# Optimization experiments

Measured on AMD Instinct MI355X. Metric: run time of the kernel, lower is better.

Reference implementation:

```python
import jax, jax.numpy as jnp
import numpy as np

D_MODEL = 2048
NUM_HEADS = 16
D_K = D_MODEL // NUM_HEADS


def setup_inputs() -> dict:
    key = jax.random.key(0)
    ks = jax.random.split(key, 9)
    s = 1.0 / np.sqrt(D_MODEL)
    return {
        "x": jax.random.normal(ks[0], (2, 2048, D_MODEL), dtype=jnp.float32),
        "Wq": jax.random.normal(ks[1], (D_MODEL, D_MODEL), dtype=jnp.float32) * s,
        "bq": jax.random.normal(ks[2], (D_MODEL,), dtype=jnp.float32) * 0.01,
        "Wk": jax.random.normal(ks[3], (D_MODEL, D_MODEL), dtype=jnp.float32) * s,
        "bk": jax.random.normal(ks[4], (D_MODEL,), dtype=jnp.float32) * 0.01,
        "Wv": jax.random.normal(ks[5], (D_MODEL, D_MODEL), dtype=jnp.float32) * s,
        "bv": jax.random.normal(ks[6], (D_MODEL,), dtype=jnp.float32) * 0.01,
        "Wo": jax.random.normal(ks[7], (D_MODEL, D_MODEL), dtype=jnp.float32) * s,
        "bo": jax.random.normal(ks[8], (D_MODEL,), dtype=jnp.float32) * 0.01,
    }


def reference(x, Wq, bq, Wk, bk, Wv, bv, Wo, bo):
    B, T, C = x.shape
    H, Dk = NUM_HEADS, D_K
    # projections (torch Linear: y = x @ W^T + b; here weights stored as [in,out])
    q = (x @ Wq + bq).reshape(B, T, H, Dk).transpose(0, 2, 1, 3)  # [B,H,T,Dk]
    k = (x @ Wk + bk).reshape(B, T, H, Dk).transpose(0, 2, 1, 3)
    v = (x @ Wv + bv).reshape(B, T, H, Dk).transpose(0, 2, 1, 3)
    score = jnp.einsum("bhqd,bhkd->bhqk", q, k) / jnp.sqrt(jnp.float32(Dk))
    attn = jax.nn.softmax(score, axis=-1)
    out = jnp.einsum("bhqk,bhkd->bhqd", attn, v)  # [B,H,T,Dk]
    out = out.transpose(0, 2, 1, 3).reshape(B, T, C)
    return out @ Wo + bo
```

## Files before the change

kernel.cpp:

```cpp
#include <hip/hip_runtime.h>
#include <cstdint>

typedef _Float16 f16;
typedef __attribute__((ext_vector_type(4))) _Float16 f16x4;
typedef __attribute__((ext_vector_type(8))) _Float16 f16x8;
typedef __attribute__((ext_vector_type(4))) float f32x4;

#define DM   2048
#define TSEQ 2048
#define NB   2
#define NH   16
#define DKH  128
#define LOG2E 1.44269504088896f

__device__ __forceinline__ void gload_lds16(const void* g, void* l) {
  __builtin_amdgcn_global_load_lds((const __attribute__((address_space(1))) void*)g,
                                   (__attribute__((address_space(3))) void*)l, 16, 0, 0);
}

#define SBAR()   asm volatile("s_barrier" ::: "memory")
#define LGKM0()  { asm volatile("s_waitcnt lgkmcnt(0)" ::: "memory"); __builtin_amdgcn_sched_barrier(0); }
#define LGKM8()  asm volatile("s_waitcnt lgkmcnt(8)" ::: "memory")
#define VMCNT4() asm volatile("s_waitcnt vmcnt(4)" ::: "memory")

__global__ __launch_bounds__(256) void cvt_kernel(const float* __restrict__ src,
                                                  f16* __restrict__ dst, int n8) {
  int i = blockIdx.x * 256 + threadIdx.x;
  if (i >= n8) return;
  const float4* s = (const float4*)src + 2 * (size_t)i;
  float4 a = s[0], b = s[1];
  f16x8 o;
  o[0]=(f16)a.x; o[1]=(f16)a.y; o[2]=(f16)a.z; o[3]=(f16)a.w;
  o[4]=(f16)b.x; o[5]=(f16)b.y; o[6]=(f16)b.z; o[7]=(f16)b.w;
  ((f16x8*)dst)[i] = o;
}

__global__ __launch_bounds__(256) void wt_kernel(const float* __restrict__ W0, const float* __restrict__ W1,
                                                 const float* __restrict__ W2, const float* __restrict__ W3,
                                                 f16* __restrict__ Dqkv, f16* __restrict__ Dout) {
  __shared__ f16 S[64 * 80];
  int z = blockIdx.z;
  const float* W = (z == 0) ? W0 : (z == 1) ? W1 : (z == 2) ? W2 : W3;
  f16* D = (z < 3) ? (Dqkv + (size_t)z * DM * DM) : Dout;
  int n0 = blockIdx.x * 64, k0 = blockIdx.y * 64;
  int tid = threadIdx.x;
#pragma unroll
  for (int i = 0; i < 4; i++) {
    int flat = i * 256 + tid;
    int r = flat >> 4, c4 = flat & 15;
    float4 v = *(const float4*)(W + (size_t)(k0 + r) * DM + n0 + c4 * 4);
    S[(c4 * 4 + 0) * 80 + r] = (f16)v.x;
    S[(c4 * 4 + 1) * 80 + r] = (f16)v.y;
    S[(c4 * 4 + 2) * 80 + r] = (f16)v.z;
    S[(c4 * 4 + 3) * 80 + r] = (f16)v.w;
  }
  __syncthreads();
#pragma unroll
  for (int i = 0; i < 2; i++) {
    int flat = i * 256 + tid;
    int nl = flat >> 3, kc = flat & 7;
    f16x8 v = *(const f16x8*)&S[nl * 80 + kc * 8];
    *(f16x8*)(D + (size_t)(n0 + nl) * DM + k0 + kc * 8) = v;
  }
}

template <int MODE>
__global__ __launch_bounds__(512, 2) void gemm_kernel(const f16* __restrict__ A, const f16* __restrict__ Bt,
                                                      const float* __restrict__ b0, const float* __restrict__ b1,
                                                      const float* __restrict__ b2,
                                                      f16* __restrict__ Oh, float* __restrict__ Of) {
  __shared__ __align__(16) f16 As[2][256 * 64];
  __shared__ __align__(16) f16 Bs[2][256 * 64];
  const int K = DM;
  const int NT = K / 64;
  const int NITER = NT / 2;
  constexpr int CPX = (MODE == 0) ? 48 : 16;
  int tid = threadIdx.x, l = tid & 63, w = tid >> 6;
  int lo = l & 15, hi = l >> 4;
  int wm = w >> 2, wn = w & 3;
  int lin = blockIdx.x;
  int swz = (lin & 7) * CPX + (lin >> 3);
  int by = swz & 15, bx = swz >> 4;
  int m0 = by * 256, n0 = bx * 256;

  const f16* Ag = A + (size_t)m0 * K;
  const f16* Bg = Bt + (size_t)n0 * K;

  auto stageA = [&](int b, int h, int t) {
#pragma unroll
    for (int i = 0; i < 2; i++) {
      int flat = i * 512 + tid;
      int row = flat >> 3, c = flat & 7;
      int csw = c ^ (row & 7);
      gload_lds16(Ag + (size_t)(h * 128 + row) * K + t * 64 + csw * 8,
                  &As[b][h * 8192 + i * 4096 + w * 512]);
    }
  };
  auto stageB = [&](int b, int h, int t) {
#pragma unroll
    for (int i = 0; i < 2; i++) {
      int flat = i * 512 + tid;
      int row = flat >> 3, c = flat & 7;
      int csw = c ^ (row & 7);
      gload_lds16(Bg + (size_t)(h * 128 + row) * K + t * 64 + csw * 8,
                  &Bs[b][h * 8192 + i * 4096 + w * 512]);
    }
  };

  f32x4 acc[8][4] = {};
  f16x8 bfr[4][2];
  f16x8 af[2][2];

#define READ_BFRAGS(b)                                                              \
  {                                                                                 \
    _Pragma("unroll")                                                               \
    for (int ni = 0; ni < 4; ni++) {                                                \
      int row = wn * 64 + ni * 16 + lo;                                             \
      bfr[ni][0] = *(const f16x8*)&Bs[b][row * 64 + (((0 + hi) ^ (row & 7)) << 3)]; \
      bfr[ni][1] = *(const f16x8*)&Bs[b][row * 64 + (((4 + hi) ^ (row & 7)) << 3)]; \
    }                                                                               \
  }

#define READ_AFRAGS(b, q)                                                           \
  {                                                                                 \
    _Pragma("unroll")                                                               \
    for (int e = 0; e < 2; e++) {                                                   \
      int row = wm * 128 + ((q) * 2 + e) * 16 + lo;                                 \
      af[e][0] = *(const f16x8*)&As[b][row * 64 + (((0 + hi) ^ (row & 7)) << 3)];   \
      af[e][1] = *(const f16x8*)&As[b][row * 64 + (((4 + hi) ^ (row & 7)) << 3)];   \
    }                                                                               \
  }

#define MFMA_Q(q)                                                                   \
    __builtin_amdgcn_s_setprio(1);                                                  \
    _Pragma("unroll")                                                               \
    for (int e = 0; e < 2; e++)                                                     \
      _Pragma("unroll")                                                             \
      for (int ni = 0; ni < 4; ni++) {                                              \
        acc[(q)*2+e][ni] = __builtin_amdgcn_mfma_f32_16x16x32_f16(af[e][0], bfr[ni][0], acc[(q)*2+e][ni], 0, 0, 0); \
        acc[(q)*2+e][ni] = __builtin_amdgcn_mfma_f32_16x16x32_f16(af[e][1], bfr[ni][1], acc[(q)*2+e][ni], 0, 0, 0); \
      }                                                                             \
    __builtin_amdgcn_s_setprio(0);

  stageB(0, 0, 0); stageB(0, 1, 0);
  stageA(0, 0, 0); stageA(0, 1, 0);
  stageB(1, 0, 1); stageB(1, 1, 1);
  VMCNT4();
  SBAR();

#pragma unroll 1
  for (int it = 0; it < NITER; ++it) {
    int T1 = 2 * it + 1;
    int t2 = (2 * it + 2 < NT) ? 2 * it + 2 : NT - 1;
    int t3 = (2 * it + 3 < NT) ? 2 * it + 3 : NT - 1;

    {
      READ_BFRAGS(0); READ_AFRAGS(0, 0);
      stageA(1, 0, T1);
      LGKM8();
      SBAR(); LGKM0(); MFMA_Q(0); SBAR();
    }
    {
      READ_AFRAGS(0, 1);
      stageA(1, 1, T1); stageB(0, 0, t2);
      SBAR(); LGKM0(); MFMA_Q(1); SBAR();
    }
    {
      READ_AFRAGS(0, 2);
      stageB(0, 1, t2);
      SBAR(); LGKM0(); MFMA_Q(2); SBAR();
    }
    {
      READ_AFRAGS(0, 3);
      SBAR(); LGKM0(); MFMA_Q(3);
      VMCNT4();
      SBAR();
    }
    {
      READ_BFRAGS(1); READ_AFRAGS(1, 0);
      stageA(0, 0, t2);
      LGKM8();
      SBAR(); LGKM0(); MFMA_Q(0); SBAR();
    }
    {
      READ_AFRAGS(1, 1);
      stageA(0, 1, t2);
      SBAR(); LGKM0(); MFMA_Q(1); SBAR();
    }
    {
      READ_AFRAGS(1, 2);
      stageB(1, 0, t3);
      SBAR(); LGKM0(); MFMA_Q(2); SBAR();
    }
    {
      READ_AFRAGS(1, 3);
      stageB(1, 1, t3);
      SBAR(); LGKM0(); MFMA_Q(3);
      VMCNT4();
      SBAR();
    }
  }
  asm volatile("s_waitcnt vmcnt(0)" ::: "memory");

#pragma unroll
  for (int mi = 0; mi < 8; mi++) {
    int gm = m0 + wm * 128 + mi * 16 + (hi << 2);
#pragma unroll
    for (int ni = 0; ni < 4; ni++) {
      int gn = n0 + wn * 64 + ni * 16 + lo;
      if (MODE == 0) {
        int proj = gn >> 11, nn = gn & 2047;
        const float* bp = (proj == 0) ? b0 : (proj == 1) ? b1 : b2;
        float bias = bp[nn];
        int h = nn >> 7, d = nn & 127;
        int b = gm >> 11;
        int t0 = gm & 2047;
        if (proj < 2) {
#pragma unroll
          for (int r = 0; r < 4; r++) {
            Oh[(size_t)proj * ((size_t)NB * NH * TSEQ * DKH) +
               (((size_t)(b * NH + h) * TSEQ + t0 + r) * DKH) + d] = (f16)(acc[mi][ni][r] + bias);
          }
        } else {
          f16x4 pk;
#pragma unroll
          for (int r = 0; r < 4; r++) pk[r] = (f16)(acc[mi][ni][r] + bias);
          *(f16x4*)(Oh + 2ull * ((size_t)NB * NH * TSEQ * DKH) +
                    ((size_t)(b * NH + h) * DKH + d) * TSEQ + t0) = pk;
        }
      } else {
        float bias = b0[gn];
#pragma unroll
        for (int r = 0; r < 4; r++)
          Of[(size_t)(gm + r) * DM + gn] = acc[mi][ni][r] + bias;
      }
    }
  }
#undef READ_BFRAGS
#undef READ_AFRAGS
#undef MFMA_Q
}

__global__ __launch_bounds__(256, 2) void attn_kernel(const f16* __restrict__ Qb, const f16* __restrict__ Kb,
                                                      const f16* __restrict__ Vtb, f16* __restrict__ AO) {
  __shared__ f16 Ks[64 * 128];
  __shared__ f16 Vt[128 * 64];
  __shared__ f16 Ps[4][32 * 72];
  int tid = threadIdx.x, l = tid & 63, w = tid >> 6;
  int lo = l & 15, hi = l >> 4;
  int lin = blockIdx.x;
  int xcd = lin & 7, slot = lin >> 3;
  int bh = xcd * 4 + (slot & 3), qt = slot >> 2;
  const float CSC = 0.12753257f;
  const float THR = 62.0f;
  const f16* Qg = Qb + (size_t)bh * TSEQ * DKH;
  const f16* Kg = Kb + (size_t)bh * TSEQ * DKH;
  const f16* Vg = Vtb + (size_t)bh * DKH * TSEQ;

  f16x8 aq[2][4];
#pragma unroll
  for (int hf = 0; hf < 2; hf++) {
    int qrow = qt * 128 + w * 32 + hf * 16 + lo;
#pragma unroll
    for (int c = 0; c < 4; c++)
      aq[hf][c] = *(const f16x8*)(Qg + (size_t)qrow * DKH + c * 32 + (hi << 3));
  }

  f32x4 o[2][8] = {};
  float mrow[2] = {-INFINITY, -INFINITY};
  float lrow[2] = {0.f, 0.f};

  for (int ktile = 0; ktile < TSEQ / 64; ++ktile) {
    __syncthreads();
#pragma unroll
    for (int i = 0; i < 4; i++) {
      int chunk = (w * 4 + i) * 64 + l;
      int rowk = chunk >> 4, c = chunk & 15;
      int csw = c ^ (rowk & 15);
      gload_lds16(Kg + (size_t)(ktile * 64 + rowk) * DKH + csw * 8, &Ks[(w * 4 + i) * 512]);
    }
#pragma unroll
    for (int i = 0; i < 4; i++) {
      int chunk = (w * 4 + i) * 64 + l;
      int d = chunk >> 3, c = chunk & 7;
      int csw = c ^ (d & 7);
      gload_lds16(Vg + (size_t)d * TSEQ + ktile * 64 + csw * 8, &Vt[(w * 4 + i) * 512]);
    }
    __syncthreads();

    f32x4 s[2][4] = {};
    __builtin_amdgcn_s_setprio(1);
#pragma unroll
    for (int ks = 0; ks < 4; ++ks) {
      int ktl = ks * 16 + lo;
#pragma unroll
      for (int c = 0; c < 4; c++) {
        int cc = (c * 4 + hi) ^ lo;
        f16x8 bk = *(const f16x8*)&Ks[ktl * 128 + cc * 8];
        s[0][ks] = __builtin_amdgcn_mfma_f32_16x16x32_f16(bk, aq[0][c], s[0][ks], 0, 0, 0);
        s[1][ks] = __builtin_amdgcn_mfma_f32_16x16x32_f16(bk, aq[1][c], s[1][ks], 0, 0, 0);
      }
    }
    __builtin_amdgcn_s_setprio(0);

#pragma unroll
    for (int hf = 0; hf < 2; hf++) {
      float mk[4];
#pragma unroll
      for (int ks = 0; ks < 4; ks++)
        mk[ks] = fmaxf(fmaxf(s[hf][ks][0], s[hf][ks][1]), fmaxf(s[hf][ks][2], s[hf][ks][3]));
      float mt = fmaxf(fmaxf(mk[0], mk[1]), fmaxf(mk[2], mk[3]));
      mt = fmaxf(mt, __shfl_xor(mt, 16));
      mt = fmaxf(mt, __shfl_xor(mt, 32));

      if (__any(mt > mrow[hf] + THR)) {
        float mn = fmaxf(mrow[hf], mt);
        float al = exp2f((mrow[hf] - mn) * CSC);
        mrow[hf] = mn;
        lrow[hf] *= al;
        float alr[4];
#pragma unroll
        for (int r = 0; r < 4; r++) alr[r] = __shfl(al, (hi << 2) + r);
#pragma unroll
        for (int dsub = 0; dsub < 8; dsub++)
#pragma unroll
          for (int r = 0; r < 4; r++) o[hf][dsub][r] *= alr[r];
      }

      float mCn = -mrow[hf] * CSC;
      float sum = 0.f;
#pragma unroll
      for (int ks = 0; ks < 4; ks++) {
        f16x4 pk;
        float part = 0.f;
#pragma unroll
        for (int r = 0; r < 4; r++) {
          float p = exp2f(__builtin_fmaf(s[hf][ks][r], CSC, mCn));
          pk[r] = (f16)p;
          part += p;
        }
        sum += part;
        *(f16x4*)&Ps[w][(hf * 16 + lo) * 72 + ks * 16 + (hi << 2)] = pk;
      }
      sum += __shfl_xor(sum, 16);
      sum += __shfl_xor(sum, 32);
      lrow[hf] += sum;
    }

    f16x8 pa[2][2];
#pragma unroll
    for (int hf = 0; hf < 2; hf++)
#pragma unroll
      for (int kk = 0; kk < 2; kk++)
        pa[hf][kk] = *(const f16x8*)&Ps[w][(hf * 16 + lo) * 72 + kk * 32 + (hi << 3)];
    __builtin_amdgcn_s_setprio(1);
#pragma unroll
    for (int kk = 0; kk < 2; kk++) {
#pragma unroll
      for (int dsub = 0; dsub < 8; dsub++) {
        int d = dsub * 16 + lo;
        f16x8 vf = *(const f16x8*)&Vt[d * 64 + (((kk * 4 + hi) ^ (d & 7)) << 3)];
        o[0][dsub] = __builtin_amdgcn_mfma_f32_16x16x32_f16(pa[0][kk], vf, o[0][dsub], 0, 0, 0);
        o[1][dsub] = __builtin_amdgcn_mfma_f32_16x16x32_f16(pa[1][kk], vf, o[1][dsub], 0, 0, 0);
      }
    }
    __builtin_amdgcn_s_setprio(0);
  }

  int b = bh >> 4, h = bh & 15;
#pragma unroll
  for (int hf = 0; hf < 2; hf++) {
    float inv = 1.0f / lrow[hf];
    float invr[4];
#pragma unroll
    for (int r = 0; r < 4; r++) invr[r] = __shfl(inv, (hi << 2) + r);
#pragma unroll
    for (int r = 0; r < 4; r++) {
      int t = qt * 128 + w * 32 + hf * 16 + (hi << 2) + r;
      f16* dst = AO + ((size_t)b * TSEQ + t) * DM + h * DKH;
#pragma unroll
      for (int dsub = 0; dsub < 8; dsub++)
        dst[dsub * 16 + lo] = (f16)(o[hf][dsub][r] * invr[r]);
    }
  }
}

extern "C" void kernel_launch(void* const* d_in, const int* in_sizes, int n_in,
                              void* d_out, int out_size, void* d_ws, size_t ws_size,
                              hipStream_t stream) {
  const float* x  = (const float*)d_in[0];
  const float* Wq = (const float*)d_in[1];
  const float* bq = (const float*)d_in[2];
  const float* Wk = (const float*)d_in[3];
  const float* bk = (const float*)d_in[4];
  const float* Wv = (const float*)d_in[5];
  const float* bv = (const float*)d_in[6];
  const float* Wo = (const float*)d_in[7];
  const float* bo = (const float*)d_in[8];

  f16* ws    = (f16*)d_ws;
  f16* xb    = ws;
  f16* WtQKV = ws + 8388608ull;
  f16* WtO   = ws + 20971520ull;
  f16* Q     = ws + 25165824ull;
  f16* Kp    = ws + 33554432ull;
  f16* Vp    = ws + 41943040ull;
  f16* AO    = xb;

  cvt_kernel<<<4096, 256, 0, stream>>>(x, xb, (NB * TSEQ * DM) / 8);
  wt_kernel<<<dim3(32, 32, 4), 256, 0, stream>>>(Wq, Wk, Wv, Wo, WtQKV, WtO);
  gemm_kernel<0><<<384, 512, 0, stream>>>(xb, WtQKV, bq, bk, bv, Q, nullptr);
  attn_kernel<<<512, 256, 0, stream>>>(Q, Kp, Vp, AO);
  gemm_kernel<1><<<128, 512, 0, stream>>>(AO, WtO, bo, nullptr, nullptr, nullptr, (float*)d_out);
}
```

Before: 300.6 us.

## Shrink GEMM N-tiles and restructure pipeline to load all A fragments upfront

The GEMM N-tile shrinks to 192 columns for the QKV projection and 128 for the output projection. This raises the grid to 512 and 256 blocks so more CUs get work (256 CUs on the device). The main loop now reads all A fragments for a K-tile into registers at once, and global-to-LDS staging is spread across the MFMA phases with fewer barriers and per-mode vmcnt waits. The cost is more register pressure from holding all A fragments, and a higher ratio of A loads per output element.

```diff
diff --git a/kernel.cpp b/kernel.cpp
--- a/kernel.cpp
+++ b/kernel.cpp
@@ -18,10 +18,8 @@
                                    (__attribute__((address_space(3))) void*)l, 16, 0, 0);
 }
 
-#define SBAR()   asm volatile("s_barrier" ::: "memory")
-#define LGKM0()  { asm volatile("s_waitcnt lgkmcnt(0)" ::: "memory"); __builtin_amdgcn_sched_barrier(0); }
-#define LGKM8()  asm volatile("s_waitcnt lgkmcnt(8)" ::: "memory")
-#define VMCNT4() asm volatile("s_waitcnt vmcnt(4)" ::: "memory")
+#define SBAR()  { asm volatile("s_barrier" ::: "memory"); __builtin_amdgcn_sched_barrier(0); }
+#define LGKM0() { asm volatile("s_waitcnt lgkmcnt(0)" ::: "memory"); __builtin_amdgcn_sched_barrier(0); }
 
 __global__ __launch_bounds__(256) void cvt_kernel(const float* __restrict__ src,
                                                   f16* __restrict__ dst, int n8) {
@@ -69,66 +67,64 @@
                                                       const float* __restrict__ b0, const float* __restrict__ b1,
                                                       const float* __restrict__ b2,
                                                       f16* __restrict__ Oh, float* __restrict__ Of) {
+  constexpr int BN   = (MODE == 0) ? 192 : 128;
+  constexpr int NFR  = BN / 64;
+  constexpr int WN   = BN / 4;
+  constexpr int NXB  = (MODE == 0) ? 32 : 16;
+  constexpr int CPX  = (16 * NXB) / 8;
   __shared__ __align__(16) f16 As[2][256 * 64];
-  __shared__ __align__(16) f16 Bs[2][256 * 64];
+  __shared__ __align__(16) f16 Bs[2][NFR * 64 * 64];
   const int K = DM;
   const int NT = K / 64;
   const int NITER = NT / 2;
-  constexpr int CPX = (MODE == 0) ? 48 : 16;
   int tid = threadIdx.x, l = tid & 63, w = tid >> 6;
   int lo = l & 15, hi = l >> 4;
   int wm = w >> 2, wn = w & 3;
   int lin = blockIdx.x;
   int swz = (lin & 7) * CPX + (lin >> 3);
   int by = swz & 15, bx = swz >> 4;
-  int m0 = by * 256, n0 = bx * 256;
+  int m0 = by * 256, n0 = bx * BN;
 
   const f16* Ag = A + (size_t)m0 * K;
   const f16* Bg = Bt + (size_t)n0 * K;
 
-  auto stageA = [&](int b, int h, int t) {
-#pragma unroll
-    for (int i = 0; i < 2; i++) {
-      int flat = i * 512 + tid;
-      int row = flat >> 3, c = flat & 7;
-      int csw = c ^ (row & 7);
-      gload_lds16(Ag + (size_t)(h * 128 + row) * K + t * 64 + csw * 8,
-                  &As[b][h * 8192 + i * 4096 + w * 512]);
-    }
+  auto stageAu = [&](int b, int u, int t) {
+    int rin = (w << 3) + (l >> 3);
+    int csw = (l & 7) ^ (rin & 7);
+    gload_lds16(Ag + (size_t)(u * 64 + rin) * K + t * 64 + csw * 8,
+                &As[b][u * 4096 + w * 512]);
   };
-  auto stageB = [&](int b, int h, int t) {
-#pragma unroll
-    for (int i = 0; i < 2; i++) {
-      int flat = i * 512 + tid;
-      int row = flat >> 3, c = flat & 7;
-      int csw = c ^ (row & 7);
-      gload_lds16(Bg + (size_t)(h * 128 + row) * K + t * 64 + csw * 8,
-                  &Bs[b][h * 8192 + i * 4096 + w * 512]);
-    }
+  auto stageBu = [&](int b, int u, int t) {
+    int rin = (w << 3) + (l >> 3);
+    int csw = (l & 7) ^ (rin & 7);
+    gload_lds16(Bg + (size_t)(u * 64 + rin) * K + t * 64 + csw * 8,
+                &Bs[b][u * 4096 + w * 512]);
   };
 
-  f32x4 acc[8][4] = {};
-  f16x8 bfr[4][2];
-  f16x8 af[2][2];
+  f32x4 acc[8][NFR] = {};
+  f16x8 bfr[NFR][2];
+  f16x8 af[4][2][2];
 
 #define READ_BFRAGS(b)                                                              \
   {                                                                                 \
     _Pragma("unroll")                                                               \
-    for (int ni = 0; ni < 4; ni++) {                                                \
-      int row = wn * 64 + ni * 16 + lo;                                             \
+    for (int ni = 0; ni < NFR; ni++) {                                              \
+      int row = wn * WN + ni * 16 + lo;                                             \
       bfr[ni][0] = *(const f16x8*)&Bs[b][row * 64 + (((0 + hi) ^ (row & 7)) << 3)]; \
       bfr[ni][1] = *(const f16x8*)&Bs[b][row * 64 + (((4 + hi) ^ (row & 7)) << 3)]; \
     }                                                                               \
   }
 
-#define READ_AFRAGS(b, q)                                                           \
+#define READ_AFRAGS_ALL(b)                                                          \
   {                                                                                 \
     _Pragma("unroll")                                                               \
-    for (int e = 0; e < 2; e++) {                                                   \
-      int row = wm * 128 + ((q) * 2 + e) * 16 + lo;                                 \
-      af[e][0] = *(const f16x8*)&As[b][row * 64 + (((0 + hi) ^ (row & 7)) << 3)];   \
-      af[e][1] = *(const f16x8*)&As[b][row * 64 + (((4 + hi) ^ (row & 7)) << 3)];   \
-    }                                                                               \
+    for (int q = 0; q < 4; q++)                                                     \
+      _Pragma("unroll")                                                             \
+      for (int e = 0; e < 2; e++) {                                                 \
+        int row = wm * 128 + (q * 2 + e) * 16 + lo;                                 \
+        af[q][e][0] = *(const f16x8*)&As[b][row * 64 + (((0 + hi) ^ (row & 7)) << 3)]; \
+        af[q][e][1] = *(const f16x8*)&As[b][row * 64 + (((4 + hi) ^ (row & 7)) << 3)]; \
+      }                                                                             \
   }
 
 #define MFMA_Q(q)                                                                   \
@@ -136,67 +132,78 @@
     _Pragma("unroll")                                                               \
     for (int e = 0; e < 2; e++)                                                     \
       _Pragma("unroll")                                                             \
-      for (int ni = 0; ni < 4; ni++) {                                              \
-        acc[(q)*2+e][ni] = __builtin_amdgcn_mfma_f32_16x16x32_f16(af[e][0], bfr[ni][0], acc[(q)*2+e][ni], 0, 0, 0); \
-        acc[(q)*2+e][ni] = __builtin_amdgcn_mfma_f32_16x16x32_f16(af[e][1], bfr[ni][1], acc[(q)*2+e][ni], 0, 0, 0); \
+      for (int ni = 0; ni < NFR; ni++) {                                            \
+        acc[(q)*2+e][ni] = __builtin_amdgcn_mfma_f32_16x16x32_f16(af[q][e][0], bfr[ni][0], acc[(q)*2+e][ni], 0, 0, 0); \
+        acc[(q)*2+e][ni] = __builtin_amdgcn_mfma_f32_16x16x32_f16(af[q][e][1], bfr[ni][1], acc[(q)*2+e][ni], 0, 0, 0); \
       }                                                                             \
     __builtin_amdgcn_s_setprio(0);
 
-  stageB(0, 0, 0); stageB(0, 1, 0);
-  stageA(0, 0, 0); stageA(0, 1, 0);
-  stageB(1, 0, 1); stageB(1, 1, 1);
-  VMCNT4();
+#define VMCNT_UPT()                                                                 \
+    if constexpr (MODE == 0) { asm volatile("s_waitcnt vmcnt(7)" ::: "memory"); }   \
+    else                     { asm volatile("s_waitcnt vmcnt(6)" ::: "memory"); }   \
+    __builtin_amdgcn_sched_barrier(0);
+
+#pragma unroll
+  for (int u = 0; u < 4; u++) stageAu(0, u, 0);
+#pragma unroll
+  for (int u = 0; u < NFR; u++) stageBu(0, u, 0);
+#pragma unroll
+  for (int u = 0; u < 4; u++) stageAu(1, u, 1);
+#pragma unroll
+  for (int u = 0; u < NFR; u++) stageBu(1, u, 1);
+  VMCNT_UPT();
   SBAR();
 
 #pragma unroll 1
   for (int it = 0; it < NITER; ++it) {
-    int T1 = 2 * it + 1;
     int t2 = (2 * it + 2 < NT) ? 2 * it + 2 : NT - 1;
     int t3 = (2 * it + 3 < NT) ? 2 * it + 3 : NT - 1;
 
     {
-      READ_BFRAGS(0); READ_AFRAGS(0, 0);
-      stageA(1, 0, T1);
-      LGKM8();
-      SBAR(); LGKM0(); MFMA_Q(0); SBAR();
-    }
-    {
-      READ_AFRAGS(0, 1);
-      stageA(1, 1, T1); stageB(0, 0, t2);
-      SBAR(); LGKM0(); MFMA_Q(1); SBAR();
-    }
-    {
-      READ_AFRAGS(0, 2);
-      stageB(0, 1, t2);
-      SBAR(); LGKM0(); MFMA_Q(2); SBAR();
-    }
-    {
-      READ_AFRAGS(0, 3);
-      SBAR(); LGKM0(); MFMA_Q(3);
-      VMCNT4();
-      SBAR();
-    }
-    {
-      READ_BFRAGS(1); READ_AFRAGS(1, 0);
-      stageA(0, 0, t2);
-      LGKM8();
-      SBAR(); LGKM0(); MFMA_Q(0); SBAR();
-    }
-    {
-      READ_AFRAGS(1, 1);
-      stageA(0, 1, t2);
-      SBAR(); LGKM0(); MFMA_Q(1); SBAR();
-    }
-    {
-      READ_AFRAGS(1, 2);
-      stageB(1, 0, t3);
-      SBAR(); LGKM0(); MFMA_Q(2); SBAR();
-    }
-    {
-      READ_AFRAGS(1, 3);
-      stageB(1, 1, t3);
-      SBAR(); LGKM0(); MFMA_Q(3);
-      VMCNT4();
+      READ_BFRAGS(0); READ_AFRAGS_ALL(0);
+      MFMA_Q(0);
+      SBAR();
+    }
+    {
+      MFMA_Q(1);
+      LGKM0();
+      SBAR();
+    }
+    {
+#pragma unroll
+      for (int u = 0; u < 4; u++) stageAu(0, u, t2);
+      MFMA_Q(2);
+      SBAR();
+    }
+    {
+#pragma unroll
+      for (int u = 0; u < NFR; u++) stageBu(0, u, t2);
+      MFMA_Q(3);
+      VMCNT_UPT();
+      SBAR();
+    }
+
+    {
+      READ_BFRAGS(1); READ_AFRAGS_ALL(1);
+      MFMA_Q(0);
+      SBAR();
+    }
+    {
+      MFMA_Q(1);
+      LGKM0();
+      SBAR();
+    }
+    {
+#pragma unroll
+      for (int u = 0; u < 4; u++) stageAu(1, u, t3);
+      MFMA_Q(2);
+      SBAR();
+    }
+    {
+#pragma unroll
+      for (int u = 0; u < NFR; u++) stageBu(1, u, t3);
+      MFMA_Q(3);
+      VMCNT_UPT();
       SBAR();
     }
   }
@@ -206,8 +213,8 @@
   for (int mi = 0; mi < 8; mi++) {
     int gm = m0 + wm * 128 + mi * 16 + (hi << 2);
 #pragma unroll
-    for (int ni = 0; ni < 4; ni++) {
-      int gn = n0 + wn * 64 + ni * 16 + lo;
+    for (int ni = 0; ni < NFR; ni++) {
+      int gn = n0 + wn * WN + ni * 16 + lo;
       if (MODE == 0) {
         int proj = gn >> 11, nn = gn & 2047;
         const float* bp = (proj == 0) ? b0 : (proj == 1) ? b1 : b2;
@@ -237,8 +244,9 @@
     }
   }
 #undef READ_BFRAGS
-#undef READ_AFRAGS
+#undef READ_AFRAGS_ALL
 #undef MFMA_Q
+#undef VMCNT_UPT
 }
 
 __global__ __launch_bounds__(256, 2) void attn_kernel(const f16* __restrict__ Qb, const f16* __restrict__ Kb,
@@ -409,7 +417,7 @@
 
   cvt_kernel<<<4096, 256, 0, stream>>>(x, xb, (NB * TSEQ * DM) / 8);
   wt_kernel<<<dim3(32, 32, 4), 256, 0, stream>>>(Wq, Wk, Wv, Wo, WtQKV, WtO);
-  gemm_kernel<0><<<384, 512, 0, stream>>>(xb, WtQKV, bq, bk, bv, Q, nullptr);
+  gemm_kernel<0><<<512, 512, 0, stream>>>(xb, WtQKV, bq, bk, bv, Q, nullptr);
   attn_kernel<<<512, 256, 0, stream>>>(Q, Kp, Vp, AO);
-  gemm_kernel<1><<<128, 512, 0, stream>>>(AO, WtO, bo, nullptr, nullptr, nullptr, (float*)d_out);
-}
+  gemm_kernel<1><<<256, 512, 0, stream>>>(AO, WtO, bo, nullptr, nullptr, nullptr, (float*)d_out);
+}
```

Result: faster. 266.5 us (-11.4%).
